# Performance work log

Hardware: AMD Instinct MI355X
Metric: run time of the kernel (lower is better)

The kernel has to match this reference:

```python
import jax, jax.numpy as jnp
import numpy as np

B, E, F1, F2, C = 8192, 8, 1024, 2048, 100


def setup_inputs() -> dict:
    key = jax.random.key(0)
    k = jax.random.split(key, 6)
    s1 = 1.0 / np.sqrt(F1)
    s2 = 1.0 / np.sqrt(F2)
    return {
        "domain": jax.random.randint(k[0], (B,), 0, E, dtype=jnp.int32),
        "x": jax.random.normal(k[1], (B, F1), dtype=jnp.float32),
        "W1": jax.random.normal(k[2], (E, F1, F2), dtype=jnp.float32) * s1,
        "b1": jax.random.normal(k[3], (E, F2), dtype=jnp.float32) * s1,
        "W2": jax.random.normal(k[4], (E, F2, C), dtype=jnp.float32) * s2,
        "b2": jax.random.normal(k[5], (E, C), dtype=jnp.float32) * s2,
    }


def reference(domain, x, W1, b1, W2, b2):
    # All-experts 2-layer MLP over the full batch (faithful to the torch loop,
    # expressed as batched einsums over the expert axis e).
    h = jax.nn.relu(jnp.einsum("bf,efh->beh", x, W1) + b1[None, :, :])  # [B,E,F2]
    logits = jnp.einsum("beh,ehc->bec", h, W2) + b2[None, :, :]          # [B,E,C]
    # Gather the expert selected by each sample's domain index.
    sel = jnp.take_along_axis(logits, domain[:, None, None].astype(jnp.int32), axis=1)
    sel = sel[:, 0, :]                                                    # [B,C]
    return jax.nn.softmax(sel, axis=-1)
```

## Files before the change

kernel.cpp:

```cpp
#include <hip/hip_runtime.h>
#include <math.h>

#define NB 8192
#define NE 8
#define F1 1024
#define F2 2048
#define NC 100
#define NCP 112
#define TM 128
#define BK 32
#define NKT (F1 / BK)
#define NCC (F2 / 128)
#define MAXTY 72

#define WS_CUR   17
#define WS_TYE   32
#define WS_TYR   104
#define WS_TYN   176
#define WS_ROWS  256

#define OFF_XH  ((size_t)65536)
#define SZ_X    ((size_t)NB * F1)
#define OFF_W1H (OFF_XH + 4 * SZ_X)
#define SZ_W1   ((size_t)NE * F2 * F1)
#define OFF_W2H (OFF_W1H + 4 * SZ_W1)
#define SZ_W2   ((size_t)NE * NCP * F2)

typedef float f32x4 __attribute__((ext_vector_type(4)));
typedef short s16x8 __attribute__((ext_vector_type(8)));
typedef unsigned short u16x8 __attribute__((ext_vector_type(8)));
typedef unsigned short u16x4 __attribute__((ext_vector_type(4)));

__device__ __forceinline__ unsigned short bf_hi(float f) {
    unsigned u = __float_as_uint(f);
    return (unsigned short)((u + 0x7FFFu + ((u >> 16) & 1u)) >> 16);
}
__device__ __forceinline__ float bf_up(unsigned short h) {
    return __uint_as_float(((unsigned)h) << 16);
}

typedef const __attribute__((address_space(1))) unsigned cgu;
typedef __attribute__((address_space(3))) unsigned ldu;
__device__ __forceinline__ void gl16(const void* g, void* l) {
    __builtin_amdgcn_global_load_lds((cgu*)g, (ldu*)l, 16, 0, 0);
}

__global__ __launch_bounds__(512) void k_plan(const int* __restrict__ dom, int* ws) {
    __shared__ int wh[8][8];
    const int tid = threadIdx.x, wave = tid >> 6, lane = tid & 63;
    int cnt[NE];
#pragma unroll
    for (int e = 0; e < NE; ++e) cnt[e] = 0;
    for (int i = tid; i < NB / 4; i += 512) {
        int4 d = ((const int4*)dom)[i];
        int v[4] = {d.x, d.y, d.z, d.w};
#pragma unroll
        for (int t = 0; t < 4; ++t)
#pragma unroll
            for (int e = 0; e < NE; ++e)
                cnt[e] += (int)__popcll(__ballot(v[t] == e));
    }
    if (lane == 0)
#pragma unroll
        for (int e = 0; e < NE; ++e) wh[wave][e] = cnt[e];
    __syncthreads();
    if (tid == 0) {
        int c[NE], off = 0, ty = 0;
        for (int e = 0; e < NE; ++e) {
            c[e] = 0;
            for (int w = 0; w < 8; ++w) c[e] += wh[w][e];
        }
        for (int e = 0; e < NE; ++e) {
            ws[WS_CUR + e] = off;
            int nt = (c[e] + TM - 1) / TM;
            for (int t = 0; t < nt; ++t) {
                ws[WS_TYE + ty] = e;
                ws[WS_TYR + ty] = off + t * TM;
                ws[WS_TYN + ty] = min(TM, c[e] - t * TM);
                ++ty;
            }
            off += c[e];
        }
        for (; ty < MAXTY; ++ty) ws[WS_TYN + ty] = 0;
    }
}

__global__ __launch_bounds__(256) void k_scatter(const int* __restrict__ dom, int* ws) {
    __shared__ int lh[NE], base[NE];
    const int tid = threadIdx.x;
    if (tid < NE) lh[tid] = 0;
    __syncthreads();
    const int b = blockIdx.x * 256 + tid;
    const int e = dom[b];
    const int r = atomicAdd(&lh[e], 1);
    __syncthreads();
    if (tid < NE) base[tid] = atomicAdd(&ws[WS_CUR + tid], lh[tid]);
    __syncthreads();
    ws[WS_ROWS + base[e] + r] = b;
}

__global__ void k_split_x(const float* __restrict__ x, unsigned short* __restrict__ xh) {
    unsigned short* xl = xh + SZ_X;
#pragma unroll
    for (int q = 0; q < 4; ++q) {
        size_t i = (size_t)blockIdx.x * 1024 + q * 256 + threadIdx.x;
        float4 v = *(const float4*)(x + i * 4);
        u16x4 h, l;
        float f[4] = {v.x, v.y, v.z, v.w};
#pragma unroll
        for (int t = 0; t < 4; ++t) {
            unsigned short hh = bf_hi(f[t]);
            h[t] = hh;
            l[t] = bf_hi(f[t] - bf_up(hh));
        }
        *(u16x4*)(xh + i * 4) = h;
        *(u16x4*)(xl + i * 4) = l;
    }
}

__global__ void k_split_w1t(const float* __restrict__ W1, unsigned short* __restrict__ w1h) {
    unsigned short* w1l = w1h + SZ_W1;
    __shared__ float t[64][65];
    const int e = blockIdx.z, k0 = blockIdx.y * 64, n0 = blockIdx.x * 64;
    const float* src = W1 + ((size_t)e * F1 + k0) * F2 + n0;
#pragma unroll
    for (int i = 0; i < 4; ++i) {
        int u = threadIdx.x + 256 * i;
        int k = u >> 4, n4 = (u & 15) * 4;
        float4 v = *(const float4*)(src + (size_t)k * F2 + n4);
        t[k][n4] = v.x; t[k][n4 + 1] = v.y; t[k][n4 + 2] = v.z; t[k][n4 + 3] = v.w;
    }
    __syncthreads();
#pragma unroll
    for (int i = 0; i < 2; ++i) {
        int u = threadIdx.x + 256 * i;
        int n = u >> 3, kg = u & 7;
        u16x8 hv, lv;
#pragma unroll
        for (int j = 0; j < 8; ++j) {
            float v = t[kg * 8 + j][n];
            unsigned short hh = bf_hi(v);
            hv[j] = hh;
            lv[j] = bf_hi(v - bf_up(hh));
        }
        size_t dst = ((size_t)e * F2 + n0 + n) * F1 + k0 + kg * 8;
        *(u16x8*)(w1h + dst) = hv;
        *(u16x8*)(w1l + dst) = lv;
    }
}

__global__ void k_split_w2t(const float* __restrict__ W2, unsigned short* __restrict__ w2h) {
    unsigned short* w2l = w2h + SZ_W2;
    __shared__ float t[64][NC + 1];
    const int e = blockIdx.y, k0 = blockIdx.x * 64;
    const float* src = W2 + ((size_t)e * F2 + k0) * NC;
    for (int u = threadIdx.x; u < 64 * NC; u += 256) {
        int k = u / NC, c = u - k * NC;
        t[k][c] = src[u];
    }
    __syncthreads();
#pragma unroll
    for (int i = 0; i < 4; ++i) {
        int u = threadIdx.x + 256 * i;
        if (u < NCP * 8) {
            int c = u >> 3, kg = u & 7;
            u16x8 hv, lv;
#pragma unroll
            for (int j = 0; j < 8; ++j) {
                float v = (c < NC) ? t[kg * 8 + j][c] : 0.f;
                unsigned short hh = bf_hi(v);
                hv[j] = hh;
                lv[j] = bf_hi(v - bf_up(hh));
            }
            size_t dst = ((size_t)e * NCP + c) * F2 + k0 + kg * 8;
            *(u16x8*)(w2h + dst) = hv;
            *(u16x8*)(w2l + dst) = lv;
        }
    }
}

__global__ __launch_bounds__(256, 2) void k_g1(
    const int* __restrict__ ws, const unsigned short* __restrict__ xh,
    const unsigned short* __restrict__ w1h, const unsigned short* __restrict__ w2h,
    const float* __restrict__ b1, float* __restrict__ out)
{
    __shared__ __align__(16) unsigned short sb[32768];
    __shared__ int rows[TM];
    const int tid = threadIdx.x;
    const int cc = blockIdx.x;
    const int ty = blockIdx.y;

    const int nr = ws[WS_TYN + ty];
    if (nr <= 0) return;
    const int e = ws[WS_TYE + ty];
    const int rbase = ws[WS_TYR + ty];
    if (tid < TM) rows[tid] = ws[WS_ROWS + rbase + min(tid, nr - 1)];
    __syncthreads();

    const int wave = tid >> 6, lane = tid & 63;
    const int wm = wave >> 1, wn = wave & 1;
    const int lg = lane >> 4, ln = lane & 15;
    const int l7 = ln & 7;

    const unsigned short* pA[2];
    const unsigned short* pB[2];
#pragma unroll
    for (int i = 0; i < 2; ++i) {
        int u = tid + 256 * i;
        int r = u >> 2, s = u & 3, g = s ^ (r & 3);
        pA[i] = xh + (size_t)rows[r] * F1 + g * 8;
        pB[i] = w1h + ((size_t)e * F2 + cc * 128 + r) * F1 + g * 8;
    }
    const int ldst0 = tid * 8;
    const int ldst1 = ldst0 + 2048;

    float bias[4];
#pragma unroll
    for (int nf = 0; nf < 4; ++nf)
        bias[nf] = b1[e * F2 + cc * 128 + wn * 64 + nf * 16 + ln];

    f32x4 acc[4][4];
#pragma unroll
    for (int m = 0; m < 4; ++m)
#pragma unroll
        for (int n = 0; n < 4; ++n) acc[m][n] = (f32x4){0.f, 0.f, 0.f, 0.f};

#define STAGE(kt, db)                                                          \
    {                                                                          \
        const int ko = (kt) * BK;                                              \
        const int b0 = (db) * 16384;                                           \
        gl16(pA[0] + ko,         &sb[b0 + ldst0]);                             \
        gl16(pA[1] + ko,         &sb[b0 + ldst1]);                             \
        gl16(pA[0] + SZ_X + ko,  &sb[b0 + 4096 + ldst0]);                      \
        gl16(pA[1] + SZ_X + ko,  &sb[b0 + 4096 + ldst1]);                      \
        gl16(pB[0] + ko,         &sb[b0 + 8192 + ldst0]);                      \
        gl16(pB[1] + ko,         &sb[b0 + 8192 + ldst1]);                      \
        gl16(pB[0] + SZ_W1 + ko, &sb[b0 + 12288 + ldst0]);                     \
        gl16(pB[1] + SZ_W1 + ko, &sb[b0 + 12288 + ldst1]);                     \
    }

    STAGE(0, 0);
    for (int kt = 0; kt < NKT; ++kt) {
        const int cur = kt & 1;
        if (kt + 1 < NKT) {
            STAGE(kt + 1, cur ^ 1);
            asm volatile("s_waitcnt vmcnt(8)" ::: "memory");
        } else {
            asm volatile("s_waitcnt vmcnt(0)" ::: "memory");
        }
        __builtin_amdgcn_s_barrier();
        __builtin_amdgcn_sched_barrier(0);
        const int b0 = cur * 16384;
        s16x8 ah[4], al[4];
#pragma unroll
        for (int m = 0; m < 4; ++m) {
            int r = wm * 64 + m * 16 + ln;
            int off = b0 + r * 32 + (lg ^ (r & 3)) * 8;
            ah[m] = *(const s16x8*)&sb[off];
            al[m] = *(const s16x8*)&sb[4096 + off];
        }
#pragma unroll
        for (int n = 0; n < 4; ++n) {
            int r = wn * 64 + n * 16 + ln;
            int off = b0 + 8192 + r * 32 + (lg ^ (r & 3)) * 8;
            s16x8 bh = *(const s16x8*)&sb[off];
            s16x8 bl = *(const s16x8*)&sb[4096 + off];
#pragma unroll
            for (int m = 0; m < 4; ++m) {
                acc[m][n] = __builtin_amdgcn_mfma_f32_16x16x32_bf16(ah[m], bh, acc[m][n], 0, 0, 0);
                acc[m][n] = __builtin_amdgcn_mfma_f32_16x16x32_bf16(al[m], bh, acc[m][n], 0, 0, 0);
                acc[m][n] = __builtin_amdgcn_mfma_f32_16x16x32_bf16(ah[m], bl, acc[m][n], 0, 0, 0);
            }
        }
        __builtin_amdgcn_sched_barrier(0);
        __builtin_amdgcn_s_barrier();
    }
#undef STAGE

    f32x4 acc2[2][7];
#pragma unroll
    for (int mf = 0; mf < 2; ++mf)
#pragma unroll
        for (int cf = 0; cf < 7; ++cf) acc2[mf][cf] = (f32x4){0.f, 0.f, 0.f, 0.f};

#pragma unroll
    for (int s = 0; s < 2; ++s) {
        __syncthreads();
        if (wn == s) {
#pragma unroll
            for (int m = 0; m < 4; ++m)
#pragma unroll
                for (int nf = 0; nf < 4; ++nf) {
                    const float bb = bias[nf];
                    const int k2 = nf * 16 + ln;
#pragma unroll
                    for (int reg = 0; reg < 4; ++reg) {
                        int row = wm * 64 + m * 16 + lg * 4 + reg;
                        float v = fmaxf(acc[m][nf][reg] + bb, 0.f);
                        unsigned short hh = bf_hi(v);
                        int off = row * 64 + ((k2 >> 3) ^ (row & 7)) * 8 + (k2 & 7);
                        sb[off] = hh;
                        sb[8192 + off] = bf_hi(v - bf_up(hh));
                    }
                }
        }
        for (int ch = wave; ch < 14; ch += 4) {
            int u = ch * 64 + lane;
            int c = u >> 3, g = u & 7;
            const unsigned short* src =
                w2h + ((size_t)e * NCP + c) * F2 + cc * 128 + s * 64 + ((g ^ (c & 7)) * 8);
            gl16(src,         &sb[16384 + ch * 512]);
            gl16(src + SZ_W2, &sb[24576 + ch * 512]);
        }
        __syncthreads();
#pragma unroll
        for (int kk = 0; kk < 2; ++kk) {
            const int sz = (kk * 4 + lg) ^ l7;
            s16x8 hh[2], hl[2];
#pragma unroll
            for (int mf = 0; mf < 2; ++mf) {
                int off = (wave * 32 + mf * 16 + ln) * 64 + sz * 8;
                hh[mf] = *(const s16x8*)&sb[off];
                hl[mf] = *(const s16x8*)&sb[8192 + off];
            }
#pragma unroll
            for (int cf = 0; cf < 7; ++cf) {
                int off = (cf * 16 + ln) * 64 + sz * 8;
                s16x8 wh = *(const s16x8*)&sb[16384 + off];
                s16x8 wl = *(const s16x8*)&sb[24576 + off];
#pragma unroll
                for (int mf = 0; mf < 2; ++mf) {
                    acc2[mf][cf] = __builtin_amdgcn_mfma_f32_16x16x32_bf16(hh[mf], wh, acc2[mf][cf], 0, 0, 0);
                    acc2[mf][cf] = __builtin_amdgcn_mfma_f32_16x16x32_bf16(hl[mf], wh, acc2[mf][cf], 0, 0, 0);
                    acc2[mf][cf] = __builtin_amdgcn_mfma_f32_16x16x32_bf16(hh[mf], wl, acc2[mf][cf], 0, 0, 0);
                }
            }
        }
    }

#pragma unroll
    for (int mf = 0; mf < 2; ++mf)
#pragma unroll
        for (int cf = 0; cf < 7; ++cf)
#pragma unroll
            for (int reg = 0; reg < 4; ++reg) {
                int row = wave * 32 + mf * 16 + lg * 4 + reg;
                int c = cf * 16 + ln;
                if (row < nr && c < NC)
                    atomicAdd(out + (size_t)rows[row] * NC + c, acc2[mf][cf][reg]);
            }
}

__global__ void k_sm(const int* __restrict__ dom, const float* __restrict__ b2,
                     float* __restrict__ out)
{
    const int row = blockIdx.x * 4 + (threadIdx.x >> 6);
    const int lane = threadIdx.x & 63;
    const int e = dom[row];
    float* base = out + (size_t)row * NC;
    float v0 = base[lane] + b2[e * NC + lane];
    float v1 = -1e30f;
    if (lane + 64 < NC) v1 = base[lane + 64] + b2[e * NC + lane + 64];
    float m = fmaxf(v0, v1);
#pragma unroll
    for (int s = 1; s < 64; s <<= 1) m = fmaxf(m, __shfl_xor(m, s));
    float p0 = expf(v0 - m);
    float p1 = (lane + 64 < NC) ? expf(v1 - m) : 0.f;
    float sum = p0 + p1;
#pragma unroll
    for (int s = 1; s < 64; s <<= 1) sum += __shfl_xor(sum, s);
    float inv = 1.f / sum;
    base[lane] = p0 * inv;
    if (lane + 64 < NC) base[lane + 64] = p1 * inv;
}

extern "C" void kernel_launch(void* const* d_in, const int* in_sizes, int n_in,
                              void* d_out, int out_size, void* d_ws, size_t ws_size,
                              hipStream_t stream)
{
    const int*   dom = (const int*)d_in[0];
    const float* x   = (const float*)d_in[1];
    const float* W1  = (const float*)d_in[2];
    const float* b1  = (const float*)d_in[3];
    const float* W2  = (const float*)d_in[4];
    const float* b2  = (const float*)d_in[5];
    float*       out = (float*)d_out;
    int*         ws  = (int*)d_ws;

    unsigned short* xh  = (unsigned short*)((char*)d_ws + OFF_XH);
    unsigned short* w1h = (unsigned short*)((char*)d_ws + OFF_W1H);
    unsigned short* w2h = (unsigned short*)((char*)d_ws + OFF_W2H);

    hipMemsetAsync(out, 0, (size_t)NB * NC * sizeof(float), stream);
    hipLaunchKernelGGL(k_plan,      dim3(1), dim3(512), 0, stream, dom, ws);
    hipLaunchKernelGGL(k_scatter,   dim3(NB / 256), dim3(256), 0, stream, dom, ws);
    hipLaunchKernelGGL(k_split_x,   dim3(NB * F1 / 4096), dim3(256), 0, stream, x, xh);
    hipLaunchKernelGGL(k_split_w1t, dim3(F2 / 64, F1 / 64, NE), dim3(256), 0, stream, W1, w1h);
    hipLaunchKernelGGL(k_split_w2t, dim3(F2 / 64, NE), dim3(256), 0, stream, W2, w2h);
    hipLaunchKernelGGL(k_g1,        dim3(NCC, MAXTY), dim3(256), 0, stream,
                       ws, xh, w1h, w2h, b1, out);
    hipLaunchKernelGGL(k_sm,        dim3(NB / 4), dim3(256), 0, stream, dom, b2, out);
}
```

Measured before the change: 384.8 us.

## Merge split kernels into one launch and relayout LDS tiles for conflict-free reads

Fuses the three fp32-to-bf16 hi/lo split kernels (x, W1, W2) into a single k_prep launch that dispatches on block index, removing two kernel launches and their inter-kernel gaps. It also changes the GEMM1 global-to-LDS staging mapping so each 16-row group's k-chunks land in contiguous 128-element slabs, replacing the XOR-swizzled address calculation with precomputed per-fragment offsets. This cuts address arithmetic in the inner loop, at the risk of LDS bank conflicts or less coalesced global loads with the new mapping.

```diff
diff --git a/kernel.cpp b/kernel.cpp
--- a/kernel.cpp
+++ b/kernel.cpp
@@ -99,82 +99,88 @@
     ws[WS_ROWS + base[e] + r] = b;
 }
 
-__global__ void k_split_x(const float* __restrict__ x, unsigned short* __restrict__ xh) {
-    unsigned short* xl = xh + SZ_X;
-#pragma unroll
-    for (int q = 0; q < 4; ++q) {
-        size_t i = (size_t)blockIdx.x * 1024 + q * 256 + threadIdx.x;
-        float4 v = *(const float4*)(x + i * 4);
-        u16x4 h, l;
-        float f[4] = {v.x, v.y, v.z, v.w};
-#pragma unroll
-        for (int t = 0; t < 4; ++t) {
-            unsigned short hh = bf_hi(f[t]);
-            h[t] = hh;
-            l[t] = bf_hi(f[t] - bf_up(hh));
-        }
-        *(u16x4*)(xh + i * 4) = h;
-        *(u16x4*)(xl + i * 4) = l;
-    }
-}
-
-__global__ void k_split_w1t(const float* __restrict__ W1, unsigned short* __restrict__ w1h) {
-    unsigned short* w1l = w1h + SZ_W1;
-    __shared__ float t[64][65];
-    const int e = blockIdx.z, k0 = blockIdx.y * 64, n0 = blockIdx.x * 64;
-    const float* src = W1 + ((size_t)e * F1 + k0) * F2 + n0;
-#pragma unroll
-    for (int i = 0; i < 4; ++i) {
-        int u = threadIdx.x + 256 * i;
-        int k = u >> 4, n4 = (u & 15) * 4;
-        float4 v = *(const float4*)(src + (size_t)k * F2 + n4);
-        t[k][n4] = v.x; t[k][n4 + 1] = v.y; t[k][n4 + 2] = v.z; t[k][n4 + 3] = v.w;
-    }
-    __syncthreads();
-#pragma unroll
-    for (int i = 0; i < 2; ++i) {
-        int u = threadIdx.x + 256 * i;
-        int n = u >> 3, kg = u & 7;
-        u16x8 hv, lv;
-#pragma unroll
-        for (int j = 0; j < 8; ++j) {
-            float v = t[kg * 8 + j][n];
-            unsigned short hh = bf_hi(v);
-            hv[j] = hh;
-            lv[j] = bf_hi(v - bf_up(hh));
-        }
-        size_t dst = ((size_t)e * F2 + n0 + n) * F1 + k0 + kg * 8;
-        *(u16x8*)(w1h + dst) = hv;
-        *(u16x8*)(w1l + dst) = lv;
-    }
-}
-
-__global__ void k_split_w2t(const float* __restrict__ W2, unsigned short* __restrict__ w2h) {
-    unsigned short* w2l = w2h + SZ_W2;
-    __shared__ float t[64][NC + 1];
-    const int e = blockIdx.y, k0 = blockIdx.x * 64;
-    const float* src = W2 + ((size_t)e * F2 + k0) * NC;
-    for (int u = threadIdx.x; u < 64 * NC; u += 256) {
-        int k = u / NC, c = u - k * NC;
-        t[k][c] = src[u];
-    }
-    __syncthreads();
-#pragma unroll
-    for (int i = 0; i < 4; ++i) {
-        int u = threadIdx.x + 256 * i;
-        if (u < NCP * 8) {
-            int c = u >> 3, kg = u & 7;
+__global__ __launch_bounds__(256) void k_prep(
+    const float* __restrict__ x, const float* __restrict__ W1,
+    const float* __restrict__ W2, unsigned short* __restrict__ xh,
+    unsigned short* __restrict__ w1h, unsigned short* __restrict__ w2h)
+{
+    __shared__ float t[64 * 101];
+    const int bx = blockIdx.x;
+    if (bx < 2048) {
+        unsigned short* xl = xh + SZ_X;
+#pragma unroll
+        for (int q = 0; q < 4; ++q) {
+            size_t i = (size_t)bx * 1024 + q * 256 + threadIdx.x;
+            float4 v = *(const float4*)(x + i * 4);
+            u16x4 h, l;
+            float f[4] = {v.x, v.y, v.z, v.w};
+#pragma unroll
+            for (int c = 0; c < 4; ++c) {
+                unsigned short hh = bf_hi(f[c]);
+                h[c] = hh;
+                l[c] = bf_hi(f[c] - bf_up(hh));
+            }
+            *(u16x4*)(xh + i * 4) = h;
+            *(u16x4*)(xl + i * 4) = l;
+        }
+    } else if (bx < 2048 + 4096) {
+        unsigned short* w1l = w1h + SZ_W1;
+        const int tt = bx - 2048;
+        const int e = tt >> 9, rem = tt & 511;
+        const int k0 = (rem >> 5) * 64, n0 = (rem & 31) * 64;
+        const float* src = W1 + ((size_t)e * F1 + k0) * F2 + n0;
+#pragma unroll
+        for (int i = 0; i < 4; ++i) {
+            int u = threadIdx.x + 256 * i;
+            int k = u >> 4, n4 = (u & 15) * 4;
+            float4 v = *(const float4*)(src + (size_t)k * F2 + n4);
+            t[k * 65 + n4] = v.x; t[k * 65 + n4 + 1] = v.y;
+            t[k * 65 + n4 + 2] = v.z; t[k * 65 + n4 + 3] = v.w;
+        }
+        __syncthreads();
+#pragma unroll
+        for (int i = 0; i < 2; ++i) {
+            int u = threadIdx.x + 256 * i;
+            int n = u >> 3, kg = u & 7;
             u16x8 hv, lv;
 #pragma unroll
             for (int j = 0; j < 8; ++j) {
-                float v = (c < NC) ? t[kg * 8 + j][c] : 0.f;
+                float v = t[(kg * 8 + j) * 65 + n];
                 unsigned short hh = bf_hi(v);
                 hv[j] = hh;
                 lv[j] = bf_hi(v - bf_up(hh));
             }
-            size_t dst = ((size_t)e * NCP + c) * F2 + k0 + kg * 8;
-            *(u16x8*)(w2h + dst) = hv;
-            *(u16x8*)(w2l + dst) = lv;
+            size_t dst = ((size_t)e * F2 + n0 + n) * F1 + k0 + kg * 8;
+            *(u16x8*)(w1h + dst) = hv;
+            *(u16x8*)(w1l + dst) = lv;
+        }
+    } else {
+        unsigned short* w2l = w2h + SZ_W2;
+        const int tt = bx - 6144;
+        const int e = tt >> 5, k0 = (tt & 31) * 64;
+        const float* src = W2 + ((size_t)e * F2 + k0) * NC;
+        for (int u = threadIdx.x; u < 64 * NC; u += 256) {
+            int k = u / NC, c = u - k * NC;
+            t[k * 101 + c] = src[u];
+        }
+        __syncthreads();
+#pragma unroll
+        for (int i = 0; i < 4; ++i) {
+            int u = threadIdx.x + 256 * i;
+            if (u < NCP * 8) {
+                int c = u >> 3, kg = u & 7;
+                u16x8 hv, lv;
+#pragma unroll
+                for (int j = 0; j < 8; ++j) {
+                    float v = (c < NC) ? t[(kg * 8 + j) * 101 + c] : 0.f;
+                    unsigned short hh = bf_hi(v);
+                    hv[j] = hh;
+                    lv[j] = bf_hi(v - bf_up(hh));
+                }
+                size_t dst = ((size_t)e * NCP + c) * F2 + k0 + kg * 8;
+                *(u16x8*)(w2h + dst) = hv;
+                *(u16x8*)(w2l + dst) = lv;
+            }
         }
     }
 }
@@ -207,9 +213,9 @@
 #pragma unroll
     for (int i = 0; i < 2; ++i) {
         int u = tid + 256 * i;
-        int r = u >> 2, s = u & 3, g = s ^ (r & 3);
-        pA[i] = xh + (size_t)rows[r] * F1 + g * 8;
-        pB[i] = w1h + ((size_t)e * F2 + cc * 128 + r) * F1 + g * 8;
+        int r = (u >> 6) * 16 + (u & 15), s = (u >> 4) & 3;
+        pA[i] = xh + (size_t)rows[r] * F1 + s * 8;
+        pB[i] = w1h + ((size_t)e * F2 + cc * 128 + r) * F1 + s * 8;
     }
     const int ldst0 = tid * 8;
     const int ldst1 = ldst0 + 2048;
@@ -218,6 +224,12 @@
 #pragma unroll
     for (int nf = 0; nf < 4; ++nf)
         bias[nf] = b1[e * F2 + cc * 128 + wn * 64 + nf * 16 + ln];
+
+    int aoff[4], boff[4];
+#pragma unroll
+    for (int m = 0; m < 4; ++m) aoff[m] = (wm * 4 + m) * 512 + lg * 128 + ln * 8;
+#pragma unroll
+    for (int n = 0; n < 4; ++n) boff[n] = 8192 + (wn * 4 + n) * 512 + lg * 128 + ln * 8;
 
     f32x4 acc[4][4];
 #pragma unroll
@@ -254,17 +266,13 @@
         s16x8 ah[4], al[4];
 #pragma unroll
         for (int m = 0; m < 4; ++m) {
-            int r = wm * 64 + m * 16 + ln;
-            int off = b0 + r * 32 + (lg ^ (r & 3)) * 8;
-            ah[m] = *(const s16x8*)&sb[off];
-            al[m] = *(const s16x8*)&sb[4096 + off];
+            ah[m] = *(const s16x8*)&sb[b0 + aoff[m]];
+            al[m] = *(const s16x8*)&sb[b0 + 4096 + aoff[m]];
         }
 #pragma unroll
         for (int n = 0; n < 4; ++n) {
-            int r = wn * 64 + n * 16 + ln;
-            int off = b0 + 8192 + r * 32 + (lg ^ (r & 3)) * 8;
-            s16x8 bh = *(const s16x8*)&sb[off];
-            s16x8 bl = *(const s16x8*)&sb[4096 + off];
+            s16x8 bh = *(const s16x8*)&sb[b0 + boff[n]];
+            s16x8 bl = *(const s16x8*)&sb[b0 + 4096 + boff[n]];
 #pragma unroll
             for (int m = 0; m < 4; ++m) {
                 acc[m][n] = __builtin_amdgcn_mfma_f32_16x16x32_bf16(ah[m], bh, acc[m][n], 0, 0, 0);
@@ -392,12 +400,11 @@
     unsigned short* w2h = (unsigned short*)((char*)d_ws + OFF_W2H);
 
     hipMemsetAsync(out, 0, (size_t)NB * NC * sizeof(float), stream);
-    hipLaunchKernelGGL(k_plan,      dim3(1), dim3(512), 0, stream, dom, ws);
-    hipLaunchKernelGGL(k_scatter,   dim3(NB / 256), dim3(256), 0, stream, dom, ws);
-    hipLaunchKernelGGL(k_split_x,   dim3(NB * F1 / 4096), dim3(256), 0, stream, x, xh);
-    hipLaunchKernelGGL(k_split_w1t, dim3(F2 / 64, F1 / 64, NE), dim3(256), 0, stream, W1, w1h);
-    hipLaunchKernelGGL(k_split_w2t, dim3(F2 / 64, NE), dim3(256), 0, stream, W2, w2h);
-    hipLaunchKernelGGL(k_g1,        dim3(NCC, MAXTY), dim3(256), 0, stream,
+    hipLaunchKernelGGL(k_plan,    dim3(1), dim3(512), 0, stream, dom, ws);
+    hipLaunchKernelGGL(k_scatter, dim3(NB / 256), dim3(256), 0, stream, dom, ws);
+    hipLaunchKernelGGL(k_prep,    dim3(2048 + 4096 + 256), dim3(256), 0, stream,
+                       x, W1, W2, xh, w1h, w2h);
+    hipLaunchKernelGGL(k_g1,      dim3(NCC, MAXTY), dim3(256), 0, stream,
                        ws, xh, w1h, w2h, b1, out);
-    hipLaunchKernelGGL(k_sm,        dim3(NB / 4), dim3(256), 0, stream, dom, b2, out);
-}
+    hipLaunchKernelGGL(k_sm,      dim3(NB / 4), dim3(256), 0, stream, dom, b2, out);
+}
```

Measured after the change: 412.4 us. 7.2% more time.
